# Kernel tuning notes

Hardware: AMD Instinct MI355X
Metric: run time of the kernel (lower is better)

Reference implementation:

```python
import jax, jax.numpy as jnp
import numpy as np

B, S, D_IN, D_H = 16, 4096, 512, 512

def setup_inputs() -> dict:
    key = jax.random.key(0)
    ks = jax.random.split(key, 8)
    inp = {
        "input": jax.random.normal(ks[0], (B, D_IN), dtype=jnp.float32),
        "context": jax.random.normal(ks[1], (B, S, D_IN), dtype=jnp.float32),
        "mask": jax.random.bernoulli(ks[2], 0.2, (B, S)),
        # parameters (torch nn.Linear layout: W [out,in], b [out])
        "W_in": jax.random.normal(ks[3], (D_H, D_IN), dtype=jnp.float32) / np.sqrt(D_IN),
        "b_in": jax.random.normal(ks[4], (D_H,), dtype=jnp.float32) * 0.01,
        "W_ctx": jax.random.normal(ks[5], (D_H, D_IN), dtype=jnp.float32) / np.sqrt(D_IN),
        "b_ctx": jax.random.normal(ks[6], (D_H,), dtype=jnp.float32) * 0.01,
        "v": jax.random.normal(ks[7], (D_H,), dtype=jnp.float32),
    }
    return inp


def reference(input, context, mask, W_in, b_in, W_ctx, b_ctx, v):
    # inp: [B, H] projected decoder state
    inp = input @ W_in.T + b_in
    # ctx: [B, S, H] projected context (this is what the torch code matmuls
    # with the softmax weights, i.e. hidden lives in hidden_dim space)
    ctx = context @ W_ctx.T + b_ctx
    # additive (Bahdanau) scores: v . tanh(inp + ctx) -> [B, S]
    scores = jnp.einsum("h,bsh->bs", v, jnp.tanh(inp[:, None, :] + ctx))
    # masked positions get -inf so they receive zero softmax weight
    scores = jnp.where(mask, -jnp.inf, scores)
    attn = jax.nn.softmax(scores, axis=-1)  # [B, S]
    # weighted sum of projected context: [B, H]
    hidden = jnp.einsum("bsh,bs->bh", ctx, attn)
    return hidden, attn
```

## Files before the change

kernel.cpp:

```cpp
#include <hip/hip_runtime.h>
#include <hip/hip_bf16.h>

#define B_  16
#define S_  4096
#define DIN 512
#define DH  512

typedef _Float16 f16x8 __attribute__((ext_vector_type(8)));
typedef float    f32x4 __attribute__((ext_vector_type(4)));


__device__ __forceinline__ float fast_tanh(float x) {
    float e = __expf(2.f * x);
    return 1.f - 2.f * __builtin_amdgcn_rcpf(e + 1.f);
}

__device__ __forceinline__ void gload_lds16(const void* g, void* l) {
    __builtin_amdgcn_global_load_lds(
        (const __attribute__((address_space(1))) void*)g,
        (__attribute__((address_space(3))) void*)l, 16, 0, 0);
}

__device__ __forceinline__ int mask_at(const void* mask, int isByte, int idx) {
    return isByte ? (int)((const unsigned char*)mask)[idx]
                  : ((const int*)mask)[idx];
}

__global__ __launch_bounds__(256)
void prep_kernel(const float* __restrict__ input,
                 const float* __restrict__ W_in,
                 const float* __restrict__ b_in,
                 const float* __restrict__ W_ctx,
                 const float* __restrict__ b_ctx,
                 const void*  __restrict__ mask,
                 _Float16* __restrict__ W16,
                 float* __restrict__ addv,
                 float* __restrict__ zeroRegion,
                 int* __restrict__ maskflag) {
    int blk = blockIdx.x;
    int tid = threadIdx.x;
    if (blk < 256) {
        int base = blk * 1024 + tid * 4;
        float4 wv = *(const float4*)(W_ctx + base);
        union { _Float16 f[4]; ushort4 u; } cv;
        cv.f[0] = (_Float16)wv.x; cv.f[1] = (_Float16)wv.y;
        cv.f[2] = (_Float16)wv.z; cv.f[3] = (_Float16)wv.w;
        *(ushort4*)(W16 + base) = cv.u;
    } else if (blk < 288) {
        int t = blk - 256;
        int b = t >> 1;
        int h = ((t & 1) << 8) + tid;
        __shared__ float inrow[DIN];
        inrow[tid]       = input[b * DIN + tid];
        inrow[tid + 256] = input[b * DIN + tid + 256];
        __syncthreads();
        const float* wr = W_in + (size_t)h * DIN;
        float acc = 0.f;
        for (int k = 0; k < DIN; k += 4) {
            float4 w4 = *(const float4*)(wr + k);
            acc += w4.x * inrow[k] + w4.y * inrow[k + 1]
                 + w4.z * inrow[k + 2] + w4.w * inrow[k + 3];
        }
        addv[b * DH + h] = acc + b_in[h] + b_ctx[h];
    } else if (blk == 288) {
        const uint4* m4 = (const uint4*)mask;
        unsigned int orw = 0;
#pragma unroll
        for (int it = 0; it < 16; ++it) {
            uint4 w = m4[it * 256 + tid];
            orw |= (w.x | w.y | w.z | w.w);
        }
        int found = ((orw & 0xFFFFFF00u) != 0) ? 1 : 0;
        __shared__ int f;
        if (tid == 0) f = 0;
        __syncthreads();
        if (found) atomicOr(&f, 1);
        __syncthreads();
        if (tid == 0) maskflag[0] = f;
    } else {
        int base = (blk - 289) * 4096;
#pragma unroll
        for (int it = 0; it < 16; ++it)
            zeroRegion[base + it * 256 + tid] = 0.f;
    }
}

__global__ __launch_bounds__(256)
void score_kernel(const float* __restrict__ context,
                  const _Float16* __restrict__ W16,
                  const float* __restrict__ addv,
                  const float* __restrict__ v,
                  float* __restrict__ scores) {
    __shared__ __align__(16) _Float16 As[2][4096];
    __shared__ __align__(16) _Float16 Bs[2][8192];

    const int tid  = threadIdx.x;
    const int wave = tid >> 6;
    const int lane = tid & 63;
    const int l15  = lane & 15;
    const int q    = lane >> 4;
    const int sg   = wave >> 1;
    const int ng   = wave & 1;

    const int xcd  = blockIdx.x & 7;
    const int slot = blockIdx.x >> 3;
    const int nt   = slot & 1;
    const int g    = (slot >> 1) * 8 + xcd;
    const int b    = g >> 5;
    const int st   = g & 31;
    const int s0   = st * 128;
    const int n0   = nt * 256;

    const float* ctxA = context + ((size_t)b * S_ + s0) * DIN;

    const int rowA0 = ((tid >> 6) * 16) + (tid & 15);
    const int kbA0  = ((tid >> 4) & 3) * 8;
    const int rowA1 = rowA0 + 64;
    const int kbA1  = kbA0;

#define STAGE_B(kc_, buf_)                                                     \
    {                                                                          \
        _Pragma("unroll")                                                      \
        for (int u = 0; u < 4; ++u) {                                          \
            int jn = wave * 4 + u;                                             \
            const _Float16* gp = W16 +                                         \
                (size_t)(n0 + jn * 16 + l15) * DIN + (kc_) * 32 + q * 8;       \
            gload_lds16(gp, &Bs[buf_][jn * 512]);                              \
        }                                                                      \
    }

#define LOADA(kc_, set_)                                                       \
    {                                                                          \
        const float* g0 = ctxA + (size_t)rowA0 * DIN + (kc_) * 32 + kbA0;      \
        const float* g1 = ctxA + (size_t)rowA1 * DIN + (kc_) * 32 + kbA1;      \
        set_[0] = *(const float4*)g0; set_[1] = *(const float4*)(g0 + 4);      \
        set_[2] = *(const float4*)g1; set_[3] = *(const float4*)(g1 + 4);      \
    }

#define WRITEA(set_, buf_)                                                     \
    {                                                                          \
        f16x8 h0, h1;                                                          \
        h0[0] = (_Float16)set_[0].x; h0[1] = (_Float16)set_[0].y;              \
        h0[2] = (_Float16)set_[0].z; h0[3] = (_Float16)set_[0].w;              \
        h0[4] = (_Float16)set_[1].x; h0[5] = (_Float16)set_[1].y;              \
        h0[6] = (_Float16)set_[1].z; h0[7] = (_Float16)set_[1].w;              \
        h1[0] = (_Float16)set_[2].x; h1[1] = (_Float16)set_[2].y;              \
        h1[2] = (_Float16)set_[2].z; h1[3] = (_Float16)set_[2].w;              \
        h1[4] = (_Float16)set_[3].x; h1[5] = (_Float16)set_[3].y;              \
        h1[6] = (_Float16)set_[3].z; h1[7] = (_Float16)set_[3].w;              \
        *(f16x8*)&As[buf_][tid * 8]        = h0;                               \
        *(f16x8*)&As[buf_][tid * 8 + 2048] = h1;                               \
    }

    f32x4 acc[4][8];
#pragma unroll
    for (int jm = 0; jm < 4; ++jm)
#pragma unroll
        for (int jn = 0; jn < 8; ++jn) acc[jm][jn] = (f32x4){0.f, 0.f, 0.f, 0.f};

    float4 aA[4], aB[4];

    STAGE_B(0, 0);
    LOADA(0, aA);
    WRITEA(aA, 0);
    LOADA(1, aB);
    __syncthreads();

#define STEP(kc_, buf_, ldset_, wrset_)                                        \
    {                                                                          \
        f16x8 afr[4], bfr[8];                                                  \
        _Pragma("unroll")                                                      \
        for (int jm = 0; jm < 4; ++jm)                                         \
            afr[jm] = *(const f16x8*)&As[buf_][(sg * 4 + jm) * 512 +           \
                                              q * 128 + l15 * 8];              \
        _Pragma("unroll")                                                      \
        for (int jn = 0; jn < 8; ++jn)                                         \
            bfr[jn] = *(const f16x8*)&Bs[buf_][(ng * 8 + jn) * 512 +           \
                                              q * 128 + l15 * 8];              \
        if ((kc_) + 2 < 16) LOADA((kc_) + 2, ldset_);                          \
        if ((kc_) + 1 < 16) STAGE_B((kc_) + 1, (buf_) ^ 1);                    \
        _Pragma("unroll")                                                      \
        for (int jn = 0; jn < 8; ++jn)                                         \
            _Pragma("unroll")                                                  \
            for (int jm = 0; jm < 4; ++jm)                                     \
                acc[jm][jn] = __builtin_amdgcn_mfma_f32_16x16x32_f16(          \
                    afr[jm], bfr[jn], acc[jm][jn], 0, 0, 0);                   \
        if ((kc_) + 1 < 16) WRITEA(wrset_, (buf_) ^ 1);                        \
        __syncthreads();                                                       \
    }

    for (int kp = 0; kp < 8; ++kp) {
        STEP(2 * kp,     0, aA, aB);
        STEP(2 * kp + 1, 1, aB, aA);
    }

    const float* avb = addv + b * DH;
    float rowsum[4][4] = {{0.f,0.f,0.f,0.f},{0.f,0.f,0.f,0.f},
                          {0.f,0.f,0.f,0.f},{0.f,0.f,0.f,0.f}};
#pragma unroll
    for (int jn = 0; jn < 8; ++jn) {
        int n = n0 + (ng * 8 + jn) * 16 + l15;
        float av = avb[n];
        float vv = v[n];
#pragma unroll
        for (int jm = 0; jm < 4; ++jm)
#pragma unroll
            for (int r = 0; r < 4; ++r)
                rowsum[jm][r] += vv * fast_tanh(acc[jm][jn][r] + av);
    }
#pragma unroll
    for (int jm = 0; jm < 4; ++jm)
#pragma unroll
        for (int r = 0; r < 4; ++r) {
            float s = rowsum[jm][r];
            s += __shfl_xor(s, 1, 16);
            s += __shfl_xor(s, 2, 16);
            s += __shfl_xor(s, 4, 16);
            s += __shfl_xor(s, 8, 16);
            if (l15 == 0) {
                int srow = s0 + (sg * 4 + jm) * 16 + q * 4 + r;
                atomicAdd(&scores[b * S_ + srow], s);
            }
        }
}

__global__ __launch_bounds__(256)
void attnwsum_kernel(const float* __restrict__ scores,
                     const float* __restrict__ context,
                     const void* __restrict__ mask,
                     const int* __restrict__ maskflag,
                     float* __restrict__ attn,
                     float* __restrict__ wsum) {
    __shared__ float rbuf[8];
    __shared__ int   selIdx[64];
    __shared__ float selW[64];
    __shared__ int   selCount;

    int b  = blockIdx.x >> 6;
    int c0 = (blockIdx.x & 63) * 64;
    int tid = threadIdx.x;
    int wv = tid >> 6, ln = tid & 63;
    int isByte = maskflag[0];
    const float* sr = scores + b * S_;

    float mx = -__builtin_inff();
    float vals[16];
#pragma unroll
    for (int it = 0; it < 16; ++it) {
        int s = it * 256 + tid;
        float x = mask_at(mask, isByte, b * S_ + s) ? -__builtin_inff() : sr[s];
        vals[it] = x;
        mx = fmaxf(mx, x);
    }
    for (int o = 1; o < 64; o <<= 1) mx = fmaxf(mx, __shfl_xor(mx, o, 64));
    if (ln == 0) rbuf[wv] = mx;
    __syncthreads();
    mx = fmaxf(fmaxf(rbuf[0], rbuf[1]), fmaxf(rbuf[2], rbuf[3]));

    float sum = 0.f;
#pragma unroll
    for (int it = 0; it < 16; ++it) sum += __expf(vals[it] - mx);
    for (int o = 1; o < 64; o <<= 1) sum += __shfl_xor(sum, o, 64);
    if (ln == 0) rbuf[4 + wv] = sum;
    if (tid == 0) selCount = 0;
    __syncthreads();
    float inv = 1.f / (rbuf[4] + rbuf[5] + rbuf[6] + rbuf[7]);

    if (tid < 64) {
        int s = c0 + tid;
        int idx = b * S_ + s;
        float sc = mask_at(mask, isByte, idx) ? -__builtin_inff() : sr[s];
        float p = __expf(sc - mx) * inv;
        attn[idx] = p;
        if (p > 1e-9f) {
            int k = atomicAdd(&selCount, 1);
            selIdx[k] = s;
            selW[k]  = p;
        }
    }
    __syncthreads();

    int cnt = selCount;
    if (cnt == 0) return;
    const float* cb = context + (size_t)b * S_ * DIN;
    float a00 = 0.f, a01 = 0.f, a10 = 0.f, a11 = 0.f;
    float a20 = 0.f, a21 = 0.f, a30 = 0.f, a31 = 0.f;
    int i = 0;
    for (; i + 4 <= cnt; i += 4) {
        const float* c0p = cb + (size_t)selIdx[i]     * DIN;
        const float* c1p = cb + (size_t)selIdx[i + 1] * DIN;
        const float* c2p = cb + (size_t)selIdx[i + 2] * DIN;
        const float* c3p = cb + (size_t)selIdx[i + 3] * DIN;
        float w0 = selW[i], w1 = selW[i + 1], w2 = selW[i + 2], w3 = selW[i + 3];
        a00 += w0 * c0p[tid]; a01 += w0 * c0p[tid + 256];
        a10 += w1 * c1p[tid]; a11 += w1 * c1p[tid + 256];
        a20 += w2 * c2p[tid]; a21 += w2 * c2p[tid + 256];
        a30 += w3 * c3p[tid]; a31 += w3 * c3p[tid + 256];
    }
    float acc0 = (a00 + a10) + (a20 + a30);
    float acc1 = (a01 + a11) + (a21 + a31);
    for (; i < cnt; ++i) {
        const float* cr = cb + (size_t)selIdx[i] * DIN;
        float w = selW[i];
        acc0 += w * cr[tid];
        acc1 += w * cr[tid + 256];
    }
    atomicAdd(&wsum[b * DIN + tid], acc0);
    atomicAdd(&wsum[b * DIN + tid + 256], acc1);
}

__global__ __launch_bounds__(256)
void hidden_kernel(const float* __restrict__ W_ctx,
                   const float* __restrict__ b_ctx,
                   const float* __restrict__ wsum,
                   float* __restrict__ hidden) {
    int b = blockIdx.x >> 1;
    int tid = threadIdx.x;
    int h = ((blockIdx.x & 1) << 8) + tid;
    __shared__ float wrow[DIN];
    wrow[tid]       = wsum[b * DIN + tid];
    wrow[tid + 256] = wsum[b * DIN + tid + 256];
    __syncthreads();
    const float* wr = W_ctx + (size_t)h * DIN;
    float acc = 0.f;
    for (int k = 0; k < DIN; k += 4) {
        float4 w4 = *(const float4*)(wr + k);
        acc += w4.x * wrow[k] + w4.y * wrow[k + 1]
             + w4.z * wrow[k + 2] + w4.w * wrow[k + 3];
    }
    hidden[b * DH + h] = acc + b_ctx[h];
}

extern "C" void kernel_launch(void* const* d_in, const int* in_sizes, int n_in,
                              void* d_out, int out_size, void* d_ws, size_t ws_size,
                              hipStream_t stream) {
    const float* input   = (const float*)d_in[0];
    const float* context = (const float*)d_in[1];
    const void*  mask    = d_in[2];
    const float* W_in    = (const float*)d_in[3];
    const float* b_in    = (const float*)d_in[4];
    const float* W_ctx   = (const float*)d_in[5];
    const float* b_ctx   = (const float*)d_in[6];
    const float* v       = (const float*)d_in[7];

    char* ws = (char*)d_ws;
    _Float16* W16   = (_Float16*)ws;
    float* addv     = (float*)(ws + 524288);
    float* scores   = (float*)(ws + 557056);
    float* wsum     = (float*)(ws + 819200);
    int*   maskflag = (int*)(ws + 851968);

    float* hidden = (float*)d_out;
    float* attn   = (float*)d_out + B_ * DH;

    prep_kernel<<<307, 256, 0, stream>>>(input, W_in, b_in, W_ctx, b_ctx, mask,
                                         W16, addv, scores ,
                                         maskflag);
    score_kernel<<<1024, 256, 0, stream>>>(context, W16, addv, v, scores);
    attnwsum_kernel<<<B_ * 64, 256, 0, stream>>>(scores, context, mask, maskflag,
                                                 attn, wsum);
    hidden_kernel<<<B_ * 2, 256, 0, stream>>>(W_ctx, b_ctx, wsum, hidden);
}
```

Measured before the change: 343.6 us.

## Cover full hidden width per score block and reduce scores in LDS without atomics

The score kernel now uses 512-thread blocks that each cover all 512 hidden columns for a 128-row slice, so the fp32 context tile is read and converted once instead of twice (previously two N-halves). Per-row partial scores from the four N-groups are combined in shared memory and written directly, which removes the atomicAdd traffic and the need to zero the scores buffer in the prep kernel. B-staging and A-prefetch are also issued earlier in each step. The cost is a larger LDS footprint (a 64KB B buffer), a single block per CU, and the loss of the XCD-aware block mapping.

```diff
diff --git a/kernel.cpp b/kernel.cpp
--- a/kernel.cpp
+++ b/kernel.cpp
@@ -35,7 +35,7 @@
                  const void*  __restrict__ mask,
                  _Float16* __restrict__ W16,
                  float* __restrict__ addv,
-                 float* __restrict__ zeroRegion,
+                 float* __restrict__ wsum,
                  int* __restrict__ maskflag) {
     int blk = blockIdx.x;
     int tid = threadIdx.x;
@@ -81,42 +81,35 @@
         int base = (blk - 289) * 4096;
 #pragma unroll
         for (int it = 0; it < 16; ++it)
-            zeroRegion[base + it * 256 + tid] = 0.f;
-    }
-}
-
-__global__ __launch_bounds__(256)
+            wsum[base + it * 256 + tid] = 0.f;
+    }
+}
+
+__global__ __launch_bounds__(512, 1)
 void score_kernel(const float* __restrict__ context,
                   const _Float16* __restrict__ W16,
                   const float* __restrict__ addv,
                   const float* __restrict__ v,
                   float* __restrict__ scores) {
     __shared__ __align__(16) _Float16 As[2][4096];
-    __shared__ __align__(16) _Float16 Bs[2][8192];
+    __shared__ __align__(16) _Float16 Bs[2][16384];
 
     const int tid  = threadIdx.x;
     const int wave = tid >> 6;
     const int lane = tid & 63;
     const int l15  = lane & 15;
     const int q    = lane >> 4;
-    const int sg   = wave >> 1;
-    const int ng   = wave & 1;
-
-    const int xcd  = blockIdx.x & 7;
-    const int slot = blockIdx.x >> 3;
-    const int nt   = slot & 1;
-    const int g    = (slot >> 1) * 8 + xcd;
-    const int b    = g >> 5;
-    const int st   = g & 31;
-    const int s0   = st * 128;
-    const int n0   = nt * 256;
+    const int sg   = wave >> 2;
+    const int ng   = wave & 3;
+
+    const int b  = blockIdx.x >> 5;
+    const int st = blockIdx.x & 31;
+    const int s0 = st * 128;
 
     const float* ctxA = context + ((size_t)b * S_ + s0) * DIN;
 
-    const int rowA0 = ((tid >> 6) * 16) + (tid & 15);
-    const int kbA0  = ((tid >> 4) & 3) * 8;
-    const int rowA1 = rowA0 + 64;
-    const int kbA1  = kbA0;
+    const int rowA = ((tid >> 6) * 16) + (tid & 15);
+    const int kbA  = ((tid >> 4) & 3) * 8;
 
 #define STAGE_B(kc_, buf_)                                                     \
     {                                                                          \
@@ -124,32 +117,26 @@
         for (int u = 0; u < 4; ++u) {                                          \
             int jn = wave * 4 + u;                                             \
             const _Float16* gp = W16 +                                         \
-                (size_t)(n0 + jn * 16 + l15) * DIN + (kc_) * 32 + q * 8;       \
+                (size_t)(jn * 16 + l15) * DIN + (kc_) * 32 + q * 8;            \
             gload_lds16(gp, &Bs[buf_][jn * 512]);                              \
         }                                                                      \
     }
 
 #define LOADA(kc_, set_)                                                       \
     {                                                                          \
-        const float* g0 = ctxA + (size_t)rowA0 * DIN + (kc_) * 32 + kbA0;      \
-        const float* g1 = ctxA + (size_t)rowA1 * DIN + (kc_) * 32 + kbA1;      \
-        set_[0] = *(const float4*)g0; set_[1] = *(const float4*)(g0 + 4);      \
-        set_[2] = *(const float4*)g1; set_[3] = *(const float4*)(g1 + 4);      \
+        const float* g0 = ctxA + (size_t)rowA * DIN + (kc_) * 32 + kbA;        \
+        set_[0] = *(const float4*)g0;                                          \
+        set_[1] = *(const float4*)(g0 + 4);                                    \
     }
 
 #define WRITEA(set_, buf_)                                                     \
     {                                                                          \
-        f16x8 h0, h1;                                                          \
+        f16x8 h0;                                                              \
         h0[0] = (_Float16)set_[0].x; h0[1] = (_Float16)set_[0].y;              \
         h0[2] = (_Float16)set_[0].z; h0[3] = (_Float16)set_[0].w;              \
         h0[4] = (_Float16)set_[1].x; h0[5] = (_Float16)set_[1].y;              \
         h0[6] = (_Float16)set_[1].z; h0[7] = (_Float16)set_[1].w;              \
-        h1[0] = (_Float16)set_[2].x; h1[1] = (_Float16)set_[2].y;              \
-        h1[2] = (_Float16)set_[2].z; h1[3] = (_Float16)set_[2].w;              \
-        h1[4] = (_Float16)set_[3].x; h1[5] = (_Float16)set_[3].y;              \
-        h1[6] = (_Float16)set_[3].z; h1[7] = (_Float16)set_[3].w;              \
-        *(f16x8*)&As[buf_][tid * 8]        = h0;                               \
-        *(f16x8*)&As[buf_][tid * 8 + 2048] = h1;                               \
+        *(f16x8*)&As[buf_][tid * 8] = h0;                                      \
     }
 
     f32x4 acc[4][8];
@@ -158,7 +145,7 @@
 #pragma unroll
         for (int jn = 0; jn < 8; ++jn) acc[jm][jn] = (f32x4){0.f, 0.f, 0.f, 0.f};
 
-    float4 aA[4], aB[4];
+    float4 aA[2], aB[2];
 
     STAGE_B(0, 0);
     LOADA(0, aA);
@@ -168,6 +155,8 @@
 
 #define STEP(kc_, buf_, ldset_, wrset_)                                        \
     {                                                                          \
+        if ((kc_) + 1 < 16) STAGE_B((kc_) + 1, (buf_) ^ 1);                    \
+        if ((kc_) + 2 < 16) LOADA((kc_) + 2, ldset_);                          \
         f16x8 afr[4], bfr[8];                                                  \
         _Pragma("unroll")                                                      \
         for (int jm = 0; jm < 4; ++jm)                                         \
@@ -177,8 +166,6 @@
         for (int jn = 0; jn < 8; ++jn)                                         \
             bfr[jn] = *(const f16x8*)&Bs[buf_][(ng * 8 + jn) * 512 +           \
                                               q * 128 + l15 * 8];              \
-        if ((kc_) + 2 < 16) LOADA((kc_) + 2, ldset_);                          \
-        if ((kc_) + 1 < 16) STAGE_B((kc_) + 1, (buf_) ^ 1);                    \
         _Pragma("unroll")                                                      \
         for (int jn = 0; jn < 8; ++jn)                                         \
             _Pragma("unroll")                                                  \
@@ -199,7 +186,7 @@
                           {0.f,0.f,0.f,0.f},{0.f,0.f,0.f,0.f}};
 #pragma unroll
     for (int jn = 0; jn < 8; ++jn) {
-        int n = n0 + (ng * 8 + jn) * 16 + l15;
+        int n = (ng * 8 + jn) * 16 + l15;
         float av = avb[n];
         float vv = v[n];
 #pragma unroll
@@ -208,6 +195,7 @@
             for (int r = 0; r < 4; ++r)
                 rowsum[jm][r] += vv * fast_tanh(acc[jm][jn][r] + av);
     }
+    float* sredF = (float*)&As[0][0];
 #pragma unroll
     for (int jm = 0; jm < 4; ++jm)
 #pragma unroll
@@ -218,10 +206,16 @@
             s += __shfl_xor(s, 4, 16);
             s += __shfl_xor(s, 8, 16);
             if (l15 == 0) {
-                int srow = s0 + (sg * 4 + jm) * 16 + q * 4 + r;
-                atomicAdd(&scores[b * S_ + srow], s);
+                int rowL = (sg * 4 + jm) * 16 + q * 4 + r;
+                sredF[ng * 128 + rowL] = s;
             }
         }
+    __syncthreads();
+    if (tid < 128) {
+        float out = sredF[tid] + sredF[128 + tid] +
+                    sredF[256 + tid] + sredF[384 + tid];
+        scores[b * S_ + s0 + tid] = out;
+    }
 }
 
 __global__ __launch_bounds__(256)
@@ -353,10 +347,9 @@
     float* hidden = (float*)d_out;
     float* attn   = (float*)d_out + B_ * DH;
 
-    prep_kernel<<<307, 256, 0, stream>>>(input, W_in, b_in, W_ctx, b_ctx, mask,
-                                         W16, addv, scores ,
-                                         maskflag);
-    score_kernel<<<1024, 256, 0, stream>>>(context, W16, addv, v, scores);
+    prep_kernel<<<291, 256, 0, stream>>>(input, W_in, b_in, W_ctx, b_ctx, mask,
+                                         W16, addv, wsum, maskflag);
+    score_kernel<<<512, 512, 0, stream>>>(context, W16, addv, v, scores);
     attnwsum_kernel<<<B_ * 64, 256, 0, stream>>>(scores, context, mask, maskflag,
                                                  attn, wsum);
     hidden_kernel<<<B_ * 2, 256, 0, stream>>>(W_ctx, b_ctx, wsum, hidden);
```

Result: faster. 290.4 us (-15.5%).
